# Kernel tuning notes

Measured on AMD Instinct MI355X. Metric: run time of the kernel, lower is better.

## Reference

```python
import jax, jax.numpy as jnp
import numpy as np

EMBED = 512
HEADS = 8
DIM_HEAD = 64
SCALE = DIM_HEAD ** -0.5


def setup_inputs() -> dict:
    key = jax.random.key(0)
    k1, k2, k3 = jax.random.split(key, 3)
    x = jax.random.normal(k1, (1, EMBED, 64, 64), dtype=jnp.float32)
    # nn.Linear(embed, 3*embed) weight [out, in] -> store transposed [in, out] for x @ W
    W_qkv = jax.random.normal(k2, (EMBED, 3 * EMBED), dtype=jnp.float32) * (EMBED ** -0.5)
    b_qkv = jax.random.normal(k3, (3 * EMBED,), dtype=jnp.float32) * 0.01
    return {"x": x, "W_qkv": W_qkv, "b_qkv": b_qkv}


def reference(x, W_qkv, b_qkv):
    B, E, h, w = x.shape
    N = h * w
    # [B, E, H, W] -> [B, N, E]
    xs = x.reshape(B, E, N).transpose(0, 2, 1)
    qkv = xs @ W_qkv + b_qkv                      # [B, N, 3E]
    q, k, v = jnp.split(qkv, 3, axis=-1)          # each [B, N, E]

    def heads(t):
        return t.reshape(B, N, HEADS, DIM_HEAD).transpose(0, 2, 1, 3)  # [B, H, N, dh]

    q, k, v = heads(q), heads(k), heads(v)
    # raw (non-softmax) attention scores, materialized as in the original
    attn = jnp.einsum('bhqd,bhkd->bhqk', q, k) * SCALE  # [B, H, N, N]
    coarse_attn = attn.sum(axis=-2)                     # sum over queries -> [B, H, N]
    output = jnp.einsum('bhqk,bhkd->bhqd', attn, v)     # [B, H, N, dh]
    return coarse_attn, output
```

## Files before the change

### kernel.cpp

```cpp
#include <hip/hip_runtime.h>


#define N_TOK 4096
#define EMBED 512
#define J3    1536
#define HEADS 8
#define DH    64
#define SCALE 0.125f

typedef float  floatx4  __attribute__((ext_vector_type(4)));
typedef short  shortx8  __attribute__((ext_vector_type(8)));
typedef unsigned short ushortx4 __attribute__((ext_vector_type(4)));
typedef unsigned int u32;
typedef unsigned short ushort;

__device__ inline ushort f2bf(float f) {
    union { float f; u32 u; } x; x.f = f;
    u32 r = x.u + 0x7fffu + ((x.u >> 16) & 1u);
    return (ushort)(r >> 16);
}
__device__ inline float bf2f(ushort u) {
    union { u32 u; float f; } x; x.u = ((u32)u) << 16; return x.f;
}
__device__ static inline void async_copy16(void* lds, const void* g) {
    auto* gp = (const __attribute__((address_space(1))) u32*)g;
    auto* lp = (__attribute__((address_space(3))) u32*)lds;
    __builtin_amdgcn_global_load_lds(gp, lp, 16, 0, 0);
}
__device__ inline int permj(int j) {
    if (j < 512) return j;
    if (j < 1024) return 512 + ((j - 512) >> 6) * 128 + ((j - 512) & 63);
    return 512 + ((j - 1024) >> 6) * 128 + 64 + ((j - 1024) & 63);
}

__global__ __launch_bounds__(256) void prep(const float* __restrict__ x,
                                            const float* __restrict__ W,
                                            ushort* __restrict__ xT,
                                            ushort* __restrict__ WT,
                                            float* __restrict__ xsum) {
    const int t = threadIdx.x;
    int bx = blockIdx.x;
    const bool isx = bx < 64;
    const float* src = isx ? x : W;
    const int C = isx ? N_TOK : J3;
    if (!isx) bx -= 64;
    __shared__ float T[64][65];
    __shared__ float red[256];
    const int c0 = bx * 64, r0 = blockIdx.y * 64;
    #pragma unroll
    for (int k = 0; k < 16; ++k) {
        int i = t + 256 * k; int r = i >> 6, c = i & 63;
        T[r][c] = src[(size_t)(r0 + r) * C + c0 + c];
    }
    __syncthreads();
    if (isx) {
        int row = t >> 2, seg = (t & 3) * 16;
        float s = 0.f;
        #pragma unroll
        for (int cc = 0; cc < 16; ++cc) s += T[row][seg + cc];
        red[t] = s;
    }
    #pragma unroll
    for (int k = 0; k < 4; ++k) {
        int i = t + 256 * k; int cr = i >> 4, cc4 = (i & 15) * 4;
        ushortx4 o = { f2bf(T[cc4 + 0][cr]), f2bf(T[cc4 + 1][cr]),
                       f2bf(T[cc4 + 2][cr]), f2bf(T[cc4 + 3][cr]) };
        int dr = isx ? (c0 + cr) : permj(c0 + cr);
        ushort* dst = isx ? xT : WT;
        *(ushortx4*)&dst[(size_t)dr * 512 + r0 + cc4] = o;
    }
    if (isx) {
        __syncthreads();
        if ((t & 3) == 0)
            atomicAdd(&xsum[r0 + (t >> 2)], red[t] + red[t + 1] + red[t + 2] + red[t + 3]);
    }
}

__global__ __launch_bounds__(256) void qkv_m(const ushort* __restrict__ xT,
                                             const ushort* __restrict__ WT,
                                             const float* __restrict__ bias,
                                             const float* __restrict__ xsum,
                                             ushort* __restrict__ Qb,
                                             float* __restrict__ Mp,
                                             float* __restrict__ out) {
    const int bx = blockIdx.x, ch = blockIdx.y;
    const int j0 = bx * 128, n0 = ch * 128;
    const bool iskv = bx >= 4;
    const int h = bx - 4;
    __shared__ __align__(16) char lds[34816];
    short* As = (short*)lds;
    short* Bs = (short*)(lds + 8192);
    short* Kt = (short*)lds;
    short* Vt = (short*)(lds + 17408);
    short* Qt = (short*)lds;
    __shared__ float qred[256];
    __shared__ float qs[64];
    const int t = threadIdx.x, lane = t & 63, w = t >> 6;
    const int wm = w & 1, wn = w >> 1;
    const int quad = lane >> 4, mrow = lane & 15;

    if (iskv) {
        int jl = t >> 2, seg = (t & 3) * 128;
        const ushort* wr = WT + (size_t)(h * 64 + jl) * 512 + seg;
        float qa = 0.f;
        #pragma unroll
        for (int g = 0; g < 16; ++g) {
            shortx8 wv = *(const shortx8*)(wr + g * 8);
            #pragma unroll
            for (int u = 0; u < 8; ++u)
                qa += bf2f((ushort)wv[u]) * xsum[seg + g * 8 + u];
        }
        qred[t] = qa;
        __syncthreads();
        if (t < 64)
            qs[t] = 4096.f * bias[h * 64 + t]
                  + qred[4 * t] + qred[4 * t + 1] + qred[4 * t + 2] + qred[4 * t + 3];
    }

    floatx4 acc[4][4] = {};
    for (int e0 = 0; e0 < 512; e0 += 32) {
        __syncthreads();
        #pragma unroll
        for (int s = 0; s < 2; ++s) {
            int i = t + 256 * s; int row = i >> 2, q = i & 3;
            async_copy16((char*)As + (size_t)w * 1024 + (size_t)s * 4096,
                         xT + (size_t)(n0 + row) * 512 + e0 + q * 8);
            async_copy16((char*)Bs + (size_t)w * 1024 + (size_t)s * 4096,
                         WT + (size_t)(j0 + row) * 512 + e0 + q * 8);
        }
        __syncthreads();
        shortx8 a[4], b[4];
        #pragma unroll
        for (int mi = 0; mi < 4; ++mi)
            a[mi] = *(const shortx8*)&As[(wm * 64 + mi * 16 + mrow) * 32 + quad * 8];
        #pragma unroll
        for (int ni = 0; ni < 4; ++ni)
            b[ni] = *(const shortx8*)&Bs[(wn * 64 + ni * 16 + mrow) * 32 + quad * 8];
        #pragma unroll
        for (int mi = 0; mi < 4; ++mi)
            #pragma unroll
            for (int ni = 0; ni < 4; ++ni)
                acc[mi][ni] = __builtin_amdgcn_mfma_f32_16x16x32_bf16(a[mi], b[ni], acc[mi][ni], 0, 0, 0);
    }
    __syncthreads();

    if (!iskv) {
        #pragma unroll
        for (int ni = 0; ni < 4; ++ni) {
            int cl = wn * 64 + ni * 16 + mrow;
            float bj = bias[j0 + cl];
            #pragma unroll
            for (int mi = 0; mi < 4; ++mi)
                #pragma unroll
                for (int r = 0; r < 4; ++r) {
                    int tok = wm * 64 + mi * 16 + quad * 4 + r;
                    Qt[tok * 136 + cl] = (short)f2bf(acc[mi][ni][r] + bj);
                }
        }
        __syncthreads();
        #pragma unroll
        for (int k = 0; k < 8; ++k) {
            int u = t + 256 * k; int row = u >> 4, seg = u & 15;
            *(shortx8*)(Qb + (size_t)(n0 + row) * 512 + j0 + seg * 8) =
                *(const shortx8*)&Qt[row * 136 + seg * 8];
        }
        return;
    }

    {
        short* dst = (wn == 0) ? Kt : Vt;
        const int boff = (wn == 0) ? 512 : 1024;
        float cp[16] = {};
        #pragma unroll
        for (int ni = 0; ni < 4; ++ni) {
            int dh = ni * 16 + mrow;
            float bj = bias[boff + h * 64 + dh];
            float qv = qs[dh];
            #pragma unroll
            for (int mi = 0; mi < 4; ++mi)
                #pragma unroll
                for (int r = 0; r < 4; ++r) {
                    int tok = wm * 64 + mi * 16 + quad * 4 + r;
                    float v = acc[mi][ni][r] + bj;
                    dst[dh * 136 + tok] = (short)f2bf(v);
                    if (wn == 0) cp[mi * 4 + r] += v * qv;
                }
        }
        if (wn == 0) {
            #pragma unroll
            for (int u = 0; u < 16; ++u) {
                float v = cp[u];
                v += __shfl_xor(v, 1, 64);
                v += __shfl_xor(v, 2, 64);
                v += __shfl_xor(v, 4, 64);
                v += __shfl_xor(v, 8, 64);
                cp[u] = v;
            }
            if (mrow == 0) {
                #pragma unroll
                for (int u = 0; u < 16; ++u) {
                    int tok = wm * 64 + (u >> 2) * 16 + quad * 4 + (u & 3);
                    out[h * N_TOK + n0 + tok] = cp[u] * SCALE;
                }
            }
        }
    }
    __syncthreads();
    const int dpb = (w & 1) * 32, db = (w >> 1) * 32;
    floatx4 m[2][2] = {};
    #pragma unroll
    for (int kt = 0; kt < 4; ++kt) {
        shortx8 ka[2], vb[2];
        #pragma unroll
        for (int fi = 0; fi < 2; ++fi)
            ka[fi] = *(const shortx8*)&Kt[(dpb + fi * 16 + mrow) * 136 + kt * 32 + quad * 8];
        #pragma unroll
        for (int fj = 0; fj < 2; ++fj)
            vb[fj] = *(const shortx8*)&Vt[(db + fj * 16 + mrow) * 136 + kt * 32 + quad * 8];
        #pragma unroll
        for (int fi = 0; fi < 2; ++fi)
            #pragma unroll
            for (int fj = 0; fj < 2; ++fj)
                m[fi][fj] = __builtin_amdgcn_mfma_f32_16x16x32_bf16(ka[fi], vb[fj], m[fi][fj], 0, 0, 0);
    }
    float* mp = Mp + ((size_t)h * 32 + ch) * 4096;
    #pragma unroll
    for (int fi = 0; fi < 2; ++fi)
        #pragma unroll
        for (int fj = 0; fj < 2; ++fj)
            #pragma unroll
            for (int r = 0; r < 4; ++r)
                mp[(dpb + fi * 16 + quad * 4 + r) * 64 + db + fj * 16 + mrow] = m[fi][fj][r];
}

__global__ __launch_bounds__(256) void reduce_m(const float* __restrict__ Mp,
                                                ushort* __restrict__ Mt) {
    const int h = blockIdx.x, part = blockIdx.y;
    const int t = threadIdx.x;
    __shared__ float sh[4][64];
    float s = 0.f;
    for (int c = 0; c < 32; ++c)
        s += Mp[((size_t)h * 32 + c) * 4096 + part * 256 + t];
    sh[t >> 6][t & 63] = s;
    __syncthreads();
    if (t < 64) {
        ushortx4 o = { f2bf(sh[0][t]), f2bf(sh[1][t]), f2bf(sh[2][t]), f2bf(sh[3][t]) };
        *(ushortx4*)&Mt[(size_t)h * 4096 + t * 64 + part * 4] = o;
    }
}

__global__ __launch_bounds__(64) void out_kernel(const ushort* __restrict__ Qb,
                                                 const ushort* __restrict__ Mt,
                                                 float* __restrict__ out) {
    const int h = blockIdx.x, n0 = blockIdx.y * 64;
    const int lane = threadIdx.x;
    const int quad = lane >> 4, mrow = lane & 15;
    floatx4 acc[4][4] = {};
    #pragma unroll
    for (int ks = 0; ks < 2; ++ks) {
        shortx8 a[4], b[4];
        #pragma unroll
        for (int mi = 0; mi < 4; ++mi)
            a[mi] = *(const shortx8*)(Qb + (size_t)(n0 + mi * 16 + mrow) * 512 + h * DH + ks * 32 + quad * 8);
        #pragma unroll
        for (int ni = 0; ni < 4; ++ni)
            b[ni] = *(const shortx8*)(Mt + (size_t)h * 4096 + (ni * 16 + mrow) * 64 + ks * 32 + quad * 8);
        #pragma unroll
        for (int mi = 0; mi < 4; ++mi)
            #pragma unroll
            for (int ni = 0; ni < 4; ++ni)
                acc[mi][ni] = __builtin_amdgcn_mfma_f32_16x16x32_bf16(a[mi], b[ni], acc[mi][ni], 0, 0, 0);
    }
    float* op = out + HEADS * N_TOK + (size_t)h * N_TOK * DH;
    #pragma unroll
    for (int mi = 0; mi < 4; ++mi)
        #pragma unroll
        for (int r = 0; r < 4; ++r) {
            int n = n0 + mi * 16 + quad * 4 + r;
            #pragma unroll
            for (int ni = 0; ni < 4; ++ni)
                op[(size_t)n * DH + ni * 16 + mrow] = acc[mi][ni][r] * SCALE;
        }
}

extern "C" void kernel_launch(void* const* d_in, const int* in_sizes, int n_in,
                              void* d_out, int out_size, void* d_ws, size_t ws_size,
                              hipStream_t stream) {
    const float* x = (const float*)d_in[0];
    const float* W = (const float*)d_in[1];
    const float* b = (const float*)d_in[2];
    float* out = (float*)d_out;

    ushort* xT = (ushort*)d_ws;
    ushort* WT = xT + (size_t)N_TOK * EMBED;
    ushort* Qb = WT + (size_t)J3 * EMBED;
    ushort* Mt = Qb + (size_t)N_TOK * EMBED;
    float* Mp   = (float*)(Mt + (size_t)HEADS * DH * DH);
    float* xsum = Mp + (size_t)HEADS * 32 * 4096;

    prep<<<dim3(88, 8), 256, 0, stream>>>(x, W, xT, WT, xsum);
    qkv_m<<<dim3(12, 32), 256, 0, stream>>>(xT, WT, b, xsum, Qb, Mp, out);
    reduce_m<<<dim3(8, 16), 256, 0, stream>>>(Mp, Mt);
    out_kernel<<<dim3(8, 64), 64, 0, stream>>>(Qb, Mt, out);
}
```

Baseline: 102.4 us.

## Fuse per-head M reduction into qkv_m via last-block atomic counter

Removes the separate reduce_m launch. Each head's kv block increments a per-head atomic counter after writing its partial M, and the 32nd block to finish sums the 32 partials and writes the bf16 Mt tile. The counter is zeroed inside prep. This saves one kernel launch and its gap, but the final reduction for each head now runs serially in a single block at the tail of qkv_m, which may lengthen the critical path.

```diff
diff --git a/kernel.cpp b/kernel.cpp
--- a/kernel.cpp
+++ b/kernel.cpp
@@ -37,9 +37,11 @@
                                             const float* __restrict__ W,
                                             ushort* __restrict__ xT,
                                             ushort* __restrict__ WT,
-                                            float* __restrict__ xsum) {
+                                            float* __restrict__ xsum,
+                                            int* __restrict__ cnt) {
     const int t = threadIdx.x;
     int bx = blockIdx.x;
+    if (bx == 0 && blockIdx.y == 0 && t < HEADS) cnt[t] = 0;
     const bool isx = bx < 64;
     const float* src = isx ? x : W;
     const int C = isx ? N_TOK : J3;
@@ -82,6 +84,8 @@
                                              const float* __restrict__ xsum,
                                              ushort* __restrict__ Qb,
                                              float* __restrict__ Mp,
+                                             ushort* __restrict__ Mt,
+                                             int* __restrict__ cnt,
                                              float* __restrict__ out) {
     const int bx = blockIdx.x, ch = blockIdx.y;
     const int j0 = bx * 128, n0 = ch * 128;
@@ -95,6 +99,7 @@
     short* Qt = (short*)lds;
     __shared__ float qred[256];
     __shared__ float qs[64];
+    __shared__ int lastf;
     const int t = threadIdx.x, lane = t & 63, w = t >> 6;
     const int wm = w & 1, wn = w >> 1;
     const int quad = lane >> 4, mrow = lane & 15;
@@ -231,21 +236,29 @@
             #pragma unroll
             for (int r = 0; r < 4; ++r)
                 mp[(dpb + fi * 16 + quad * 4 + r) * 64 + db + fj * 16 + mrow] = m[fi][fj][r];
-}
-
-__global__ __launch_bounds__(256) void reduce_m(const float* __restrict__ Mp,
-                                                ushort* __restrict__ Mt) {
-    const int h = blockIdx.x, part = blockIdx.y;
-    const int t = threadIdx.x;
-    __shared__ float sh[4][64];
-    float s = 0.f;
-    for (int c = 0; c < 32; ++c)
-        s += Mp[((size_t)h * 32 + c) * 4096 + part * 256 + t];
-    sh[t >> 6][t & 63] = s;
-    __syncthreads();
-    if (t < 64) {
-        ushortx4 o = { f2bf(sh[0][t]), f2bf(sh[1][t]), f2bf(sh[2][t]), f2bf(sh[3][t]) };
-        *(ushortx4*)&Mt[(size_t)h * 4096 + t * 64 + part * 4] = o;
+
+    __threadfence();
+    __syncthreads();
+    if (t == 0) {
+        int old = __hip_atomic_fetch_add(&cnt[h], 1, __ATOMIC_ACQ_REL, __HIP_MEMORY_SCOPE_AGENT);
+        lastf = (old == 31);
+    }
+    __syncthreads();
+    if (lastf) {
+        for (int part = 0; part < 16; ++part) {
+            float s = 0.f;
+            #pragma unroll 4
+            for (int c = 0; c < 32; ++c)
+                s += Mp[((size_t)h * 32 + c) * 4096 + part * 256 + t];
+            __syncthreads();
+            qred[t] = s;
+            __syncthreads();
+            if (t < 64) {
+                ushortx4 o = { f2bf(qred[t]), f2bf(qred[64 + t]),
+                               f2bf(qred[128 + t]), f2bf(qred[192 + t]) };
+                *(ushortx4*)&Mt[(size_t)h * 4096 + t * 64 + part * 4] = o;
+            }
+        }
     }
 }
 
@@ -297,9 +310,9 @@
     ushort* Mt = Qb + (size_t)N_TOK * EMBED;
     float* Mp   = (float*)(Mt + (size_t)HEADS * DH * DH);
     float* xsum = Mp + (size_t)HEADS * 32 * 4096;
-
-    prep<<<dim3(88, 8), 256, 0, stream>>>(x, W, xT, WT, xsum);
-    qkv_m<<<dim3(12, 32), 256, 0, stream>>>(xT, WT, b, xsum, Qb, Mp, out);
-    reduce_m<<<dim3(8, 16), 256, 0, stream>>>(Mp, Mt);
+    int*   cnt  = (int*)(xsum + 512);
+
+    prep<<<dim3(88, 8), 256, 0, stream>>>(x, W, xT, WT, xsum, cnt);
+    qkv_m<<<dim3(12, 32), 256, 0, stream>>>(xT, WT, b, xsum, Qb, Mp, Mt, cnt, out);
     out_kernel<<<dim3(8, 64), 64, 0, stream>>>(Qb, Mt, out);
 }
```

After: 175.9 us. +71.8%, slower.
